# Kernel tuning notes

Measured on AMD Instinct MI355X. Metric: run time of the kernel, lower is better.

The kernel has to match this reference:

```python
import jax, jax.numpy as jnp
import numpy as np

N_NODES = 50000
NUM_FEATURE = 256
NUM_HIDDEN = 128
NUM_CLASSES = 16
N_EDGES = 1600000


def gcn_conv(x, W, b, src, dst, deg_inv_sqrt, n_nodes):
    # GCNConv: h = x @ W ; out[i] = sum_{j->i} norm_ji * h[j] + b
    # with symmetric normalization over the self-loop-augmented graph.
    h = x @ W  # [N, out_ch]
    norm = deg_inv_sqrt[src] * deg_inv_sqrt[dst]  # [E']
    msgs = h[src] * norm[:, None]  # [E', out_ch] (dominant intermediate)
    out = jax.ops.segment_sum(msgs, dst, num_segments=n_nodes)
    return out + b


def setup_inputs() -> dict:
    key = jax.random.key(0)
    k_x, k_e, k_w1, k_b1, k_w2, k_b2 = jax.random.split(key, 6)
    x = jax.random.normal(k_x, (N_NODES, NUM_FEATURE), dtype=jnp.float32)
    edge_index = jax.random.randint(k_e, (2, N_EDGES), 0, N_NODES, dtype=jnp.int64)
    # Glorot init like PyG's GCNConv linear
    s1 = (6.0 / (NUM_FEATURE + NUM_HIDDEN)) ** 0.5
    s2 = (6.0 / (NUM_HIDDEN + NUM_CLASSES)) ** 0.5
    W1 = jax.random.uniform(k_w1, (NUM_FEATURE, NUM_HIDDEN), jnp.float32, -s1, s1)
    b1 = jnp.zeros((NUM_HIDDEN,), jnp.float32)
    W2 = jax.random.uniform(k_w2, (NUM_HIDDEN, NUM_CLASSES), jnp.float32, -s2, s2)
    b2 = jnp.zeros((NUM_CLASSES,), jnp.float32)
    return {"x": x, "edge_index": edge_index, "W1": W1, "b1": b1, "W2": W2, "b2": b2}


def reference(x, edge_index, W1, b1, W2, b2):
    n = x.shape[0]
    # add self-loops (done inside GCNConv for each layer; identical both times)
    loops = jnp.arange(n, dtype=edge_index.dtype)
    src = jnp.concatenate([edge_index[0], loops])
    dst = jnp.concatenate([edge_index[1], loops])
    deg = jax.ops.segment_sum(jnp.ones_like(dst, dtype=x.dtype), dst, num_segments=n)
    deg_inv_sqrt = jnp.where(deg > 0, jax.lax.rsqrt(deg), 0.0)

    h = jax.nn.relu(gcn_conv(x, W1, b1, src, dst, deg_inv_sqrt, n))
    # F.dropout with training=False is the identity (eval-mode baseline)
    logits = gcn_conv(h, W2, b2, src, dst, deg_inv_sqrt, n)
    return jax.nn.log_softmax(logits, axis=1)
```

## Files before the change

kernel.cpp:

```cpp
#include <hip/hip_runtime.h>
#include <hip/hip_fp16.h>
#include <math.h>

#define NF 256
#define NH 128
#define NC 16
#define NB 391
#define NBLK 512

typedef __attribute__((ext_vector_type(8))) short bf16x8;
typedef __attribute__((ext_vector_type(4))) float f32x4;
typedef __attribute__((ext_vector_type(2))) float f32v2;

__device__ __forceinline__ unsigned f2b(float f) {
    unsigned u = __float_as_uint(f);
    return (u + 0x7FFFu + ((u >> 16) & 1u)) >> 16;
}
__device__ __forceinline__ unsigned packt(float a, float b) {
    return (__float_as_uint(a) >> 16) | (__float_as_uint(b) & 0xFFFF0000u);
}
union h2u { __half2 h; unsigned u; };
__device__ __forceinline__ __half2 uh(unsigned u) { h2u c; c.u = u; return c.h; }
__device__ __forceinline__ unsigned hu(__half2 h) { h2u c; c.h = h; return c.u; }

__global__ void prep_kernel(const int* __restrict__ dst, int* __restrict__ hist, int E,
                            const float* __restrict__ W1, unsigned short* __restrict__ W1T,
                            unsigned* __restrict__ h1c32, unsigned* __restrict__ h2sb,
                            int N) {
    __shared__ int h[NB];
    int b = blockIdx.x, tid = threadIdx.x;
    if (b < NBLK) {
        for (int i = tid; i < NB; i += 256) h[i] = 0;
        __syncthreads();
        int e0 = (int)((long long)b * E / NBLK), e1 = (int)((long long)(b + 1) * E / NBLK);
        for (int e = e0 + tid; e < e1; e += 256)
            atomicAdd(&h[dst[e] >> 7], 1);
        __syncthreads();
        for (int i = tid; i < NB; i += 256) hist[b * NB + i] = h[i];
    } else {
        int idx = (b - NBLK) * 256 + tid;
        int n = idx >> 8, k = idx & 255;
        W1T[n * 256 + k] = (unsigned short)f2b(W1[(size_t)k * NH + n]);
        if (idx < 32) {
            int q = idx >> 4, j = idx & 15;
            h1c32[(size_t)q * (N + 1) * 16 + (size_t)N * 16 + j] = 0u;
        } else if (idx < 40) {
            h2sb[(size_t)N * 8 + (idx - 32)] = 0u;
        }
    }
}

__global__ void scanR_kernel(const int* __restrict__ hist, int* __restrict__ bsum) {
    __shared__ int sm[NBLK];
    int k = blockIdx.x, t = threadIdx.x;
    sm[t] = hist[t * NB + k];
    __syncthreads();
    for (int off = NBLK / 2; off > 0; off >>= 1) {
        if (t < off) sm[t] += sm[t + off];
        __syncthreads();
    }
    if (t == 0) bsum[k] = sm[0];
}

__global__ void scanB_kernel(const int* __restrict__ bsum, int* __restrict__ ubase,
                             int* __restrict__ pbase, int N, int E) {
    __shared__ int smu[512];
    __shared__ int smp[512];
    int t = threadIdx.x;
    int vu = (t < NB) ? bsum[t] : 0;
    int vp = (t < NB) ? (((vu + 7) & ~7) + 904) : 0;
    smu[t] = vu; smp[t] = vp;
    __syncthreads();
    for (int off = 1; off < 512; off <<= 1) {
        int uu = (t >= off) ? smu[t - off] : 0;
        int pp = (t >= off) ? smp[t - off] : 0;
        __syncthreads();
        smu[t] += uu; smp[t] += pp;
        __syncthreads();
    }
    if (t < NB) { ubase[t] = smu[t] - vu; pbase[t] = smp[t] - vp; }
    if (t == 0) ubase[NB] = E;
}

__global__ void scanC_kernel(int* __restrict__ hist, const int* __restrict__ ubase) {
    __shared__ int sm[NBLK];
    int k = blockIdx.x, t = threadIdx.x;
    int v = hist[t * NB + k];
    sm[t] = v;
    __syncthreads();
    for (int off = 1; off < NBLK; off <<= 1) {
        int u = (t >= off) ? sm[t - off] : 0;
        __syncthreads();
        sm[t] += u;
        __syncthreads();
    }
    hist[t * NB + k] = ubase[k] + sm[t] - v;
}

__global__ void passB_kernel(const int* __restrict__ src, const int* __restrict__ dst,
                             const int* __restrict__ hist, unsigned* __restrict__ ebuf,
                             int E) {
    __shared__ int cur[NB];
    int b = blockIdx.x;
    for (int i = threadIdx.x; i < NB; i += 256) cur[i] = hist[b * NB + i];
    __syncthreads();
    int e0 = (int)((long long)b * E / NBLK), e1 = (int)((long long)(b + 1) * E / NBLK);
    for (int e = e0 + (int)threadIdx.x; e < e1; e += 256) {
        int d = dst[e];
        int pos = atomicAdd(&cur[d >> 7], 1);
        ebuf[pos] = ((unsigned)d << 16) | (unsigned)src[e];
    }
}

__global__ void passC_kernel(const unsigned* __restrict__ ebuf, const int* __restrict__ ubase,
                             const int* __restrict__ pbase, int* __restrict__ rowptr,
                             int* __restrict__ degs, float* __restrict__ dis,
                             unsigned short* __restrict__ colidx, int N) {
    __shared__ int h[128];
    __shared__ int s2[128];
    __shared__ int curp[128];
    int k = blockIdx.x, t = threadIdx.x;
    if (t < 128) h[t] = 0;
    __syncthreads();
    int e0 = ubase[k], e1 = ubase[k + 1];
    for (int e = e0 + t; e < e1; e += 256)
        atomicAdd(&h[(ebuf[e] >> 16) & 127], 1);
    __syncthreads();
    int v = (t < 128) ? h[t] : 0;
    int pd = (v + 7) & ~7;
    if (t < 128) s2[t] = pd;
    __syncthreads();
    for (int off = 1; off < 128; off <<= 1) {
        int u = (t < 128 && t >= off) ? s2[t - off] : 0;
        __syncthreads();
        if (t < 128) s2[t] += u;
        __syncthreads();
    }
    if (t < 128) {
        int start = pbase[k] + s2[t] - pd;
        int node = k * 128 + t;
        if (node < N) {
            rowptr[node] = start;
            degs[node] = v;
            dis[node] = rsqrtf((float)(v + 1));
        }
        curp[t] = start;
    }
    __syncthreads();
    for (int e = e0 + t; e < e1; e += 256) {
        unsigned w = ebuf[e];
        int dl = (w >> 16) & 127;
        int pos = atomicAdd(&curp[dl], 1);
        colidx[pos] = (unsigned short)(w & 0xFFFFu);
    }
    __syncthreads();
    if (t < 128) {
        int endp = pbase[k] + s2[t];
        for (int q = curp[t]; q < endp; ++q) colidx[q] = (unsigned short)N;
    }
}

__global__ __launch_bounds__(256) void gemm1_mfma_kernel(
    const float* __restrict__ x, const unsigned short* __restrict__ W1T,
    const float* __restrict__ dis, unsigned char* __restrict__ h1c, int N) {
    __shared__ char sx[32768];
    int tid = threadIdx.x;
    int wid = tid >> 6, lane = tid & 63;

    for (int it = 0; it < 8; ++it) {
        int lr = it * 4 + wid;
        int grow = blockIdx.x * 32 + lr;
        if (grow >= N) grow = N - 1;
        int fsw = (lr & 7) << 1;
        const char* gp = (const char*)x + (size_t)grow * 1024 + ((lane ^ fsw) << 4);
        __builtin_amdgcn_global_load_lds(gp, sx + lr * 1024 + lane * 16, 16, 0, 0);
    }
    __syncthreads();

    int lrow = lane & 15, lk = lane >> 4;
    int rt = wid & 1, nh = wid >> 1;
    int lr = rt * 16 + lrow;
    int fr = (lr & 7) << 1;
    const float4* lds4 = (const float4*)sx;

    bf16x8 a[8];
#pragma unroll
    for (int kk = 0; kk < 8; ++kk) {
        int v = (kk * 8 + lk * 2) ^ fr;
        float4 lo = lds4[lr * 64 + v];
        float4 hi = lds4[lr * 64 + v + 1];
        union { unsigned u[4]; bf16x8 vv; } av;
        av.u[0] = packt(lo.x, lo.y);
        av.u[1] = packt(lo.z, lo.w);
        av.u[2] = packt(hi.x, hi.y);
        av.u[3] = packt(hi.z, hi.w);
        a[kk] = av.vv;
    }

    f32x4 acc[4];
#pragma unroll
    for (int t = 0; t < 4; ++t) acc[t] = (f32x4){0.f, 0.f, 0.f, 0.f};

#pragma unroll
    for (int nt = 0; nt < 4; ++nt) {
        int n = nh * 64 + nt * 16 + lrow;
        const unsigned short* wp = W1T + (size_t)n * 256 + lk * 8;
        bf16x8 b0 = *(const bf16x8*)(wp + 0 * 32);
        bf16x8 b1 = *(const bf16x8*)(wp + 1 * 32);
        bf16x8 b2 = *(const bf16x8*)(wp + 2 * 32);
        bf16x8 b3 = *(const bf16x8*)(wp + 3 * 32);
        bf16x8 b4 = *(const bf16x8*)(wp + 4 * 32);
        bf16x8 b5 = *(const bf16x8*)(wp + 5 * 32);
        bf16x8 b6 = *(const bf16x8*)(wp + 6 * 32);
        bf16x8 b7 = *(const bf16x8*)(wp + 7 * 32);
        acc[nt] = __builtin_amdgcn_mfma_f32_16x16x32_bf16(a[0], b0, acc[nt], 0, 0, 0);
        acc[nt] = __builtin_amdgcn_mfma_f32_16x16x32_bf16(a[1], b1, acc[nt], 0, 0, 0);
        acc[nt] = __builtin_amdgcn_mfma_f32_16x16x32_bf16(a[2], b2, acc[nt], 0, 0, 0);
        acc[nt] = __builtin_amdgcn_mfma_f32_16x16x32_bf16(a[3], b3, acc[nt], 0, 0, 0);
        acc[nt] = __builtin_amdgcn_mfma_f32_16x16x32_bf16(a[4], b4, acc[nt], 0, 0, 0);
        acc[nt] = __builtin_amdgcn_mfma_f32_16x16x32_bf16(a[5], b5, acc[nt], 0, 0, 0);
        acc[nt] = __builtin_amdgcn_mfma_f32_16x16x32_bf16(a[6], b6, acc[nt], 0, 0, 0);
        acc[nt] = __builtin_amdgcn_mfma_f32_16x16x32_bf16(a[7], b7, acc[nt], 0, 0, 0);
    }

    int rb = blockIdx.x * 32;
    int crow0 = rb + rt * 16 + lk * 4;
#pragma unroll
    for (int r = 0; r < 4; ++r) {
        int row = crow0 + r;
        if (row < N) {
            float dr = dis[row];
            size_t base = ((size_t)nh * (N + 1) + row) * 64;
#pragma unroll
            for (int nt = 0; nt < 4; ++nt) {
                float v = acc[nt][r] * dr;
                int pk = __builtin_amdgcn_cvt_pk_fp8_f32(v, v, 0, 0);
                h1c[base + nt * 16 + lrow] = (unsigned char)(pk & 0xFF);
            }
        }
    }
}

__global__ __launch_bounds__(256) void aggall_kernel(
    const int* __restrict__ rowptr, const int* __restrict__ degs,
    const unsigned short* __restrict__ colidx,
    const unsigned char* __restrict__ h1c, __half2* __restrict__ aggT, int N, int bps) {
    int p = blockIdx.x / bps;
    int i = (blockIdx.x - p * bps) * 16 + (threadIdx.x >> 4);
    if (i >= N) return;
    int l = threadIdx.x & 15;
    const unsigned* slab = (const unsigned*)(h1c + (size_t)p * (N + 1) * 64);
    unsigned sv = slab[(size_t)i * 16 + l];
    f32v2 c0 = __builtin_amdgcn_cvt_pk_f32_fp8((int)sv, 0);
    f32v2 c1 = __builtin_amdgcn_cvt_pk_f32_fp8((int)sv, 1);
    float f0 = c0.x, f1 = c0.y, f2 = c1.x, f3 = c1.y;
    int e = rowptr[i];
    int cnt8 = (degs[i] + 7) >> 3;
    if (cnt8 > 0) {
        uint4 w = *reinterpret_cast<const uint4*>(colidx + e);
        for (int b = 1; b < cnt8; ++b) {
            uint4 wn = *reinterpret_cast<const uint4*>(colidx + e + 8 * b);
            int a0 = w.x & 0xFFFF, a1 = w.x >> 16, a2 = w.y & 0xFFFF, a3 = w.y >> 16;
            int a4 = w.z & 0xFFFF, a5 = w.z >> 16, a6 = w.w & 0xFFFF, a7 = w.w >> 16;
            unsigned g0 = slab[(size_t)a0 * 16 + l];
            unsigned g1 = slab[(size_t)a1 * 16 + l];
            unsigned g2 = slab[(size_t)a2 * 16 + l];
            unsigned g3 = slab[(size_t)a3 * 16 + l];
            unsigned g4 = slab[(size_t)a4 * 16 + l];
            unsigned g5 = slab[(size_t)a5 * 16 + l];
            unsigned g6 = slab[(size_t)a6 * 16 + l];
            unsigned g7 = slab[(size_t)a7 * 16 + l];
            f32v2 d;
            d = __builtin_amdgcn_cvt_pk_f32_fp8((int)g0, 0); f0 += d.x; f1 += d.y;
            d = __builtin_amdgcn_cvt_pk_f32_fp8((int)g0, 1); f2 += d.x; f3 += d.y;
            d = __builtin_amdgcn_cvt_pk_f32_fp8((int)g1, 0); f0 += d.x; f1 += d.y;
            d = __builtin_amdgcn_cvt_pk_f32_fp8((int)g1, 1); f2 += d.x; f3 += d.y;
            d = __builtin_amdgcn_cvt_pk_f32_fp8((int)g2, 0); f0 += d.x; f1 += d.y;
            d = __builtin_amdgcn_cvt_pk_f32_fp8((int)g2, 1); f2 += d.x; f3 += d.y;
            d = __builtin_amdgcn_cvt_pk_f32_fp8((int)g3, 0); f0 += d.x; f1 += d.y;
            d = __builtin_amdgcn_cvt_pk_f32_fp8((int)g3, 1); f2 += d.x; f3 += d.y;
            d = __builtin_amdgcn_cvt_pk_f32_fp8((int)g4, 0); f0 += d.x; f1 += d.y;
            d = __builtin_amdgcn_cvt_pk_f32_fp8((int)g4, 1); f2 += d.x; f3 += d.y;
            d = __builtin_amdgcn_cvt_pk_f32_fp8((int)g5, 0); f0 += d.x; f1 += d.y;
            d = __builtin_amdgcn_cvt_pk_f32_fp8((int)g5, 1); f2 += d.x; f3 += d.y;
            d = __builtin_amdgcn_cvt_pk_f32_fp8((int)g6, 0); f0 += d.x; f1 += d.y;
            d = __builtin_amdgcn_cvt_pk_f32_fp8((int)g6, 1); f2 += d.x; f3 += d.y;
            d = __builtin_amdgcn_cvt_pk_f32_fp8((int)g7, 0); f0 += d.x; f1 += d.y;
            d = __builtin_amdgcn_cvt_pk_f32_fp8((int)g7, 1); f2 += d.x; f3 += d.y;
            w = wn;
        }
        {
            int a0 = w.x & 0xFFFF, a1 = w.x >> 16, a2 = w.y & 0xFFFF, a3 = w.y >> 16;
            int a4 = w.z & 0xFFFF, a5 = w.z >> 16, a6 = w.w & 0xFFFF, a7 = w.w >> 16;
            unsigned g0 = slab[(size_t)a0 * 16 + l];
            unsigned g1 = slab[(size_t)a1 * 16 + l];
            unsigned g2 = slab[(size_t)a2 * 16 + l];
            unsigned g3 = slab[(size_t)a3 * 16 + l];
            unsigned g4 = slab[(size_t)a4 * 16 + l];
            unsigned g5 = slab[(size_t)a5 * 16 + l];
            unsigned g6 = slab[(size_t)a6 * 16 + l];
            unsigned g7 = slab[(size_t)a7 * 16 + l];
            f32v2 d;
            d = __builtin_amdgcn_cvt_pk_f32_fp8((int)g0, 0); f0 += d.x; f1 += d.y;
            d = __builtin_amdgcn_cvt_pk_f32_fp8((int)g0, 1); f2 += d.x; f3 += d.y;
            d = __builtin_amdgcn_cvt_pk_f32_fp8((int)g1, 0); f0 += d.x; f1 += d.y;
            d = __builtin_amdgcn_cvt_pk_f32_fp8((int)g1, 1); f2 += d.x; f3 += d.y;
            d = __builtin_amdgcn_cvt_pk_f32_fp8((int)g2, 0); f0 += d.x; f1 += d.y;
            d = __builtin_amdgcn_cvt_pk_f32_fp8((int)g2, 1); f2 += d.x; f3 += d.y;
            d = __builtin_amdgcn_cvt_pk_f32_fp8((int)g3, 0); f0 += d.x; f1 += d.y;
            d = __builtin_amdgcn_cvt_pk_f32_fp8((int)g3, 1); f2 += d.x; f3 += d.y;
            d = __builtin_amdgcn_cvt_pk_f32_fp8((int)g4, 0); f0 += d.x; f1 += d.y;
            d = __builtin_amdgcn_cvt_pk_f32_fp8((int)g4, 1); f2 += d.x; f3 += d.y;
            d = __builtin_amdgcn_cvt_pk_f32_fp8((int)g5, 0); f0 += d.x; f1 += d.y;
            d = __builtin_amdgcn_cvt_pk_f32_fp8((int)g5, 1); f2 += d.x; f3 += d.y;
            d = __builtin_amdgcn_cvt_pk_f32_fp8((int)g6, 0); f0 += d.x; f1 += d.y;
            d = __builtin_amdgcn_cvt_pk_f32_fp8((int)g6, 1); f2 += d.x; f3 += d.y;
            d = __builtin_amdgcn_cvt_pk_f32_fp8((int)g7, 0); f0 += d.x; f1 += d.y;
            d = __builtin_amdgcn_cvt_pk_f32_fp8((int)g7, 1); f2 += d.x; f3 += d.y;
        }
    }
    __half2 h01 = __floats2half2_rn(f0, f1);
    __half2 h23 = __floats2half2_rn(f2, f3);
    size_t base = ((size_t)(p * 2 + (l >> 3)) * N + i) * 16 + ((2 * l) & 15);
    *reinterpret_cast<uint2*>(aggT + base) = make_uint2(hu(h01), hu(h23));
}

__global__ __launch_bounds__(256) void relu_gemm2_kernel(
    const __half2* __restrict__ aggT, const float* __restrict__ dis,
    const float* __restrict__ b1, const float* __restrict__ W2,
    __half2* __restrict__ h2sb, int N) {
    __shared__ float sW2[NH * NC];
    __shared__ float srow[4][NH];
    int tid = threadIdx.x;
    for (int k = tid; k < NH * NC; k += 256) sW2[k] = W2[k];
    __syncthreads();

    int wid = tid >> 6, lane = tid & 63;
    int i = blockIdx.x * 4 + wid;
    if (i >= N) return;
    int p = lane >> 4, l16 = lane & 15;
    float2 f = __half22float2(aggT[((size_t)p * N + i) * 16 + l16]);
    float di = dis[i];
    int c0 = p * 32 + l16 * 2;
    srow[wid][c0]     = fmaxf(di * f.x + b1[c0], 0.f);
    srow[wid][c0 + 1] = fmaxf(di * f.y + b1[c0 + 1], 0.f);
    int j = lane & 15, q = lane >> 4;
    const float* rw = srow[wid];
    float pacc = 0.f;
#pragma unroll
    for (int cc = 0; cc < 32; ++cc) {
        int c = q * 32 + cc;
        pacc += rw[c] * sW2[c * NC + j];
    }
    pacc += __shfl_xor(pacc, 16, 64);
    pacc += __shfl_xor(pacc, 32, 64);
    float dp = di * pacc;
    float plo = __shfl(dp, (lane << 1) & 63, 64);
    float phi = __shfl(dp, ((lane << 1) | 1) & 63, 64);
    if (lane < 8) h2sb[(size_t)i * 8 + lane] = __floats2half2_rn(plo, phi);
}

__global__ void layer2_kernel(const int* __restrict__ rowptr, const int* __restrict__ degs,
                              const unsigned short* __restrict__ colidx,
                              const uint2* __restrict__ h2sb2, const float* __restrict__ dis,
                              const float* __restrict__ b2, float* __restrict__ out, int N) {
    int t = blockIdx.x * 256 + threadIdx.x;
    int i = t >> 2;
    if (i >= N) return;
    int j4 = t & 3;
    int e = rowptr[i];
    int cnt4 = (degs[i] + 3) >> 2;
    uint2 sv = h2sb2[(size_t)i * 4 + j4];
    __half2 acc0 = uh(sv.x), acc1 = uh(sv.y);
    if (cnt4 > 0) {
        uint2 w = *reinterpret_cast<const uint2*>(colidx + e);
        for (int b = 1; b < cnt4; ++b) {
            uint2 wn = *reinterpret_cast<const uint2*>(colidx + e + 4 * b);
            int a0 = w.x & 0xFFFF, a1 = w.x >> 16;
            int a2 = w.y & 0xFFFF, a3 = w.y >> 16;
            uint2 g0 = h2sb2[(size_t)a0 * 4 + j4];
            uint2 g1 = h2sb2[(size_t)a1 * 4 + j4];
            uint2 g2 = h2sb2[(size_t)a2 * 4 + j4];
            uint2 g3 = h2sb2[(size_t)a3 * 4 + j4];
            acc0 = __hadd2(acc0, __hadd2(__hadd2(uh(g0.x), uh(g1.x)),
                                         __hadd2(uh(g2.x), uh(g3.x))));
            acc1 = __hadd2(acc1, __hadd2(__hadd2(uh(g0.y), uh(g1.y)),
                                         __hadd2(uh(g2.y), uh(g3.y))));
            w = wn;
        }
        int a0 = w.x & 0xFFFF, a1 = w.x >> 16;
        int a2 = w.y & 0xFFFF, a3 = w.y >> 16;
        uint2 g0 = h2sb2[(size_t)a0 * 4 + j4];
        uint2 g1 = h2sb2[(size_t)a1 * 4 + j4];
        uint2 g2 = h2sb2[(size_t)a2 * 4 + j4];
        uint2 g3 = h2sb2[(size_t)a3 * 4 + j4];
        acc0 = __hadd2(acc0, __hadd2(__hadd2(uh(g0.x), uh(g1.x)),
                                     __hadd2(uh(g2.x), uh(g3.x))));
        acc1 = __hadd2(acc1, __hadd2(__hadd2(uh(g0.y), uh(g1.y)),
                                     __hadd2(uh(g2.y), uh(g3.y))));
    }
    float2 f0 = __half22float2(acc0);
    float2 f1 = __half22float2(acc1);
    float di = dis[i];
    float4 bb = *reinterpret_cast<const float4*>(b2 + 4 * j4);
    float l0 = di * f0.x + bb.x;
    float l1 = di * f0.y + bb.y;
    float l2 = di * f1.x + bb.z;
    float l3 = di * f1.y + bb.w;
    float m = fmaxf(fmaxf(l0, l1), fmaxf(l2, l3));
    m = fmaxf(m, __shfl_xor(m, 1, 64));
    m = fmaxf(m, __shfl_xor(m, 2, 64));
    float s = __expf(l0 - m) + __expf(l1 - m) + __expf(l2 - m) + __expf(l3 - m);
    s += __shfl_xor(s, 1, 64);
    s += __shfl_xor(s, 2, 64);
    float lse = m + __logf(s);
    float4 o = make_float4(l0 - lse, l1 - lse, l2 - lse, l3 - lse);
    *reinterpret_cast<float4*>(out + (size_t)i * NC + 4 * j4) = o;
}

extern "C" void kernel_launch(void* const* d_in, const int* in_sizes, int n_in,
                              void* d_out, int out_size, void* d_ws, size_t ws_size,
                              hipStream_t stream) {
    const float* x  = (const float*)d_in[0];
    const int*   ei = (const int*)d_in[1];
    const float* W1 = (const float*)d_in[2];
    const float* b1 = (const float*)d_in[3];
    const float* W2 = (const float*)d_in[4];
    const float* b2 = (const float*)d_in[5];
    float* out = (float*)d_out;

    const int N = in_sizes[0] / NF;
    const int E = in_sizes[1] / 2;
    const int* src = ei;
    const int* dst = ei + E;

    unsigned char*  h1c    = (unsigned char*)d_ws;
    __half2*        aggT   = (__half2*)(h1c + (size_t)2 * (N + 1) * 64);
    __half2*        h2sb   = aggT + (size_t)4 * N * 16;
    float*          dis    = (float*)(h2sb + (size_t)(N + 1) * 8);
    int*            degs   = (int*)(dis + N);
    int*            rowptr = degs + N;
    int*            hist   = rowptr + N;
    int*            bsum   = hist + NBLK * NB;
    int*            ubase  = bsum + NB;
    int*            pbase  = ubase + NB + 1;
    unsigned*       ebuf   = (unsigned*)(pbase + NB + 2);
    unsigned short* colidx = (unsigned short*)(ebuf + E);
    unsigned short* W1T    = colidx + (size_t)E + 360000;

    prep_kernel<<<NBLK + 128, 256, 0, stream>>>(dst, hist, E, W1, W1T,
                                                (unsigned*)h1c, (unsigned*)h2sb, N);
    scanR_kernel<<<NB, NBLK, 0, stream>>>(hist, bsum);
    scanB_kernel<<<1, 512, 0, stream>>>(bsum, ubase, pbase, N, E);
    scanC_kernel<<<NB, NBLK, 0, stream>>>(hist, ubase);
    passB_kernel<<<NBLK, 256, 0, stream>>>(src, dst, hist, ebuf, E);
    passC_kernel<<<NB, 256, 0, stream>>>(ebuf, ubase, pbase, rowptr, degs, dis, colidx, N);

    gemm1_mfma_kernel<<<(N + 31) / 32, 256, 0, stream>>>(x, W1T, dis, h1c, N);

    const int bps = (N + 15) / 16;
    aggall_kernel<<<2 * bps, 256, 0, stream>>>(rowptr, degs, colidx, h1c, aggT, N, bps);

    relu_gemm2_kernel<<<(N + 3) / 4, 256, 0, stream>>>(aggT, dis, b1, W2, h2sb, N);

    layer2_kernel<<<((size_t)N * 4 + 255) / 256, 256, 0, stream>>>(rowptr, degs, colidx,
                                                                   (const uint2*)h2sb, dis, b2, out, N);
}
```

Baseline: 144.1 us.

## Fuse layer-1 aggregation into ReLU/GEMM2 kernel and merge scan kernels

The separate FP8 gather-aggregation kernel and the ReLU+GEMM2 kernel are fused into one kernel, so the fp16 aggT intermediate is never written to or read back from global memory. To support this, h1c is changed from two per-half slabs to an interleaved 128-byte row layout. Each wavefront handles one node, with its two 32-lane halves taking alternate edges and combining partial sums through a cross-half shuffle. The scanB and scanC kernels are also merged into one, which removes a launch; each block recomputes its own prefix with a reduction. The trade-off is less parallelism per node (one wave instead of eight lane groups split across two slabs) and redundant prefix work in every scan block.

Result: slower. 148.7 us (+3.2%).

```diff
diff --git a/kernel.cpp b/kernel.cpp
--- a/kernel.cpp
+++ b/kernel.cpp
@@ -21,12 +21,11 @@
 }
 union h2u { __half2 h; unsigned u; };
 __device__ __forceinline__ __half2 uh(unsigned u) { h2u c; c.u = u; return c.h; }
-__device__ __forceinline__ unsigned hu(__half2 h) { h2u c; c.h = h; return c.u; }
 
 __global__ void prep_kernel(const int* __restrict__ dst, int* __restrict__ hist, int E,
                             const float* __restrict__ W1, unsigned short* __restrict__ W1T,
                             unsigned* __restrict__ h1c32, unsigned* __restrict__ h2sb,
-                            int N) {
+                            int* __restrict__ ubase, int N) {
     __shared__ int h[NB];
     int b = blockIdx.x, tid = threadIdx.x;
     if (b < NBLK) {
@@ -42,10 +41,11 @@
         int n = idx >> 8, k = idx & 255;
         W1T[n * 256 + k] = (unsigned short)f2b(W1[(size_t)k * NH + n]);
         if (idx < 32) {
-            int q = idx >> 4, j = idx & 15;
-            h1c32[(size_t)q * (N + 1) * 16 + (size_t)N * 16 + j] = 0u;
+            h1c32[(size_t)N * 32 + idx] = 0u;
         } else if (idx < 40) {
             h2sb[(size_t)N * 8 + (idx - 32)] = 0u;
+        } else if (idx == 40) {
+            ubase[NB] = E;
         }
     }
 }
@@ -62,39 +62,33 @@
     if (t == 0) bsum[k] = sm[0];
 }
 
-__global__ void scanB_kernel(const int* __restrict__ bsum, int* __restrict__ ubase,
-                             int* __restrict__ pbase, int N, int E) {
-    __shared__ int smu[512];
-    __shared__ int smp[512];
-    int t = threadIdx.x;
-    int vu = (t < NB) ? bsum[t] : 0;
-    int vp = (t < NB) ? (((vu + 7) & ~7) + 904) : 0;
-    smu[t] = vu; smp[t] = vp;
-    __syncthreads();
-    for (int off = 1; off < 512; off <<= 1) {
-        int uu = (t >= off) ? smu[t - off] : 0;
-        int pp = (t >= off) ? smp[t - off] : 0;
-        __syncthreads();
-        smu[t] += uu; smp[t] += pp;
-        __syncthreads();
-    }
-    if (t < NB) { ubase[t] = smu[t] - vu; pbase[t] = smp[t] - vp; }
-    if (t == 0) ubase[NB] = E;
-}
-
-__global__ void scanC_kernel(int* __restrict__ hist, const int* __restrict__ ubase) {
-    __shared__ int sm[NBLK];
+__global__ void scanCB_kernel(const int* __restrict__ bsum, int* __restrict__ hist,
+                              int* __restrict__ ubase, int* __restrict__ pbase) {
+    __shared__ int sr[NBLK];
+    __shared__ int sp[NBLK];
+    __shared__ int ubs;
     int k = blockIdx.x, t = threadIdx.x;
+    int vu = (t < k) ? bsum[t] : 0;
+    int vp = (t < k) ? (((vu + 7) & ~7) + 904) : 0;
+    sr[t] = vu; sp[t] = vp;
+    __syncthreads();
+    for (int off = NBLK / 2; off > 0; off >>= 1) {
+        if (t < off) { sr[t] += sr[t + off]; sp[t] += sp[t + off]; }
+        __syncthreads();
+    }
+    if (t == 0) { ubs = sr[0]; ubase[k] = sr[0]; pbase[k] = sp[0]; }
+    __syncthreads();
+    int ub = ubs;
     int v = hist[t * NB + k];
-    sm[t] = v;
+    sr[t] = v;
     __syncthreads();
     for (int off = 1; off < NBLK; off <<= 1) {
-        int u = (t >= off) ? sm[t - off] : 0;
-        __syncthreads();
-        sm[t] += u;
-        __syncthreads();
-    }
-    hist[t * NB + k] = ubase[k] + sm[t] - v;
+        int u = (t >= off) ? sr[t - off] : 0;
+        __syncthreads();
+        sr[t] += u;
+        __syncthreads();
+    }
+    hist[t * NB + k] = ub + sr[t] - v;
 }
 
 __global__ void passB_kernel(const int* __restrict__ src, const int* __restrict__ dst,
@@ -230,7 +224,7 @@
         int row = crow0 + r;
         if (row < N) {
             float dr = dis[row];
-            size_t base = ((size_t)nh * (N + 1) + row) * 64;
+            size_t base = (size_t)row * 128 + nh * 64;
 #pragma unroll
             for (int nt = 0; nt < 4; ++nt) {
                 float v = acc[nt][r] * dr;
@@ -241,92 +235,10 @@
     }
 }
 
-__global__ __launch_bounds__(256) void aggall_kernel(
+__global__ __launch_bounds__(256) void aggfused_kernel(
     const int* __restrict__ rowptr, const int* __restrict__ degs,
     const unsigned short* __restrict__ colidx,
-    const unsigned char* __restrict__ h1c, __half2* __restrict__ aggT, int N, int bps) {
-    int p = blockIdx.x / bps;
-    int i = (blockIdx.x - p * bps) * 16 + (threadIdx.x >> 4);
-    if (i >= N) return;
-    int l = threadIdx.x & 15;
-    const unsigned* slab = (const unsigned*)(h1c + (size_t)p * (N + 1) * 64);
-    unsigned sv = slab[(size_t)i * 16 + l];
-    f32v2 c0 = __builtin_amdgcn_cvt_pk_f32_fp8((int)sv, 0);
-    f32v2 c1 = __builtin_amdgcn_cvt_pk_f32_fp8((int)sv, 1);
-    float f0 = c0.x, f1 = c0.y, f2 = c1.x, f3 = c1.y;
-    int e = rowptr[i];
-    int cnt8 = (degs[i] + 7) >> 3;
-    if (cnt8 > 0) {
-        uint4 w = *reinterpret_cast<const uint4*>(colidx + e);
-        for (int b = 1; b < cnt8; ++b) {
-            uint4 wn = *reinterpret_cast<const uint4*>(colidx + e + 8 * b);
-            int a0 = w.x & 0xFFFF, a1 = w.x >> 16, a2 = w.y & 0xFFFF, a3 = w.y >> 16;
-            int a4 = w.z & 0xFFFF, a5 = w.z >> 16, a6 = w.w & 0xFFFF, a7 = w.w >> 16;
-            unsigned g0 = slab[(size_t)a0 * 16 + l];
-            unsigned g1 = slab[(size_t)a1 * 16 + l];
-            unsigned g2 = slab[(size_t)a2 * 16 + l];
-            unsigned g3 = slab[(size_t)a3 * 16 + l];
-            unsigned g4 = slab[(size_t)a4 * 16 + l];
-            unsigned g5 = slab[(size_t)a5 * 16 + l];
-            unsigned g6 = slab[(size_t)a6 * 16 + l];
-            unsigned g7 = slab[(size_t)a7 * 16 + l];
-            f32v2 d;
-            d = __builtin_amdgcn_cvt_pk_f32_fp8((int)g0, 0); f0 += d.x; f1 += d.y;
-            d = __builtin_amdgcn_cvt_pk_f32_fp8((int)g0, 1); f2 += d.x; f3 += d.y;
-            d = __builtin_amdgcn_cvt_pk_f32_fp8((int)g1, 0); f0 += d.x; f1 += d.y;
-            d = __builtin_amdgcn_cvt_pk_f32_fp8((int)g1, 1); f2 += d.x; f3 += d.y;
-            d = __builtin_amdgcn_cvt_pk_f32_fp8((int)g2, 0); f0 += d.x; f1 += d.y;
-            d = __builtin_amdgcn_cvt_pk_f32_fp8((int)g2, 1); f2 += d.x; f3 += d.y;
-            d = __builtin_amdgcn_cvt_pk_f32_fp8((int)g3, 0); f0 += d.x; f1 += d.y;
-            d = __builtin_amdgcn_cvt_pk_f32_fp8((int)g3, 1); f2 += d.x; f3 += d.y;
-            d = __builtin_amdgcn_cvt_pk_f32_fp8((int)g4, 0); f0 += d.x; f1 += d.y;
-            d = __builtin_amdgcn_cvt_pk_f32_fp8((int)g4, 1); f2 += d.x; f3 += d.y;
-            d = __builtin_amdgcn_cvt_pk_f32_fp8((int)g5, 0); f0 += d.x; f1 += d.y;
-            d = __builtin_amdgcn_cvt_pk_f32_fp8((int)g5, 1); f2 += d.x; f3 += d.y;
-            d = __builtin_amdgcn_cvt_pk_f32_fp8((int)g6, 0); f0 += d.x; f1 += d.y;
-            d = __builtin_amdgcn_cvt_pk_f32_fp8((int)g6, 1); f2 += d.x; f3 += d.y;
-            d = __builtin_amdgcn_cvt_pk_f32_fp8((int)g7, 0); f0 += d.x; f1 += d.y;
-            d = __builtin_amdgcn_cvt_pk_f32_fp8((int)g7, 1); f2 += d.x; f3 += d.y;
-            w = wn;
-        }
-        {
-            int a0 = w.x & 0xFFFF, a1 = w.x >> 16, a2 = w.y & 0xFFFF, a3 = w.y >> 16;
-            int a4 = w.z & 0xFFFF, a5 = w.z >> 16, a6 = w.w & 0xFFFF, a7 = w.w >> 16;
-            unsigned g0 = slab[(size_t)a0 * 16 + l];
-            unsigned g1 = slab[(size_t)a1 * 16 + l];
-            unsigned g2 = slab[(size_t)a2 * 16 + l];
-            unsigned g3 = slab[(size_t)a3 * 16 + l];
-            unsigned g4 = slab[(size_t)a4 * 16 + l];
-            unsigned g5 = slab[(size_t)a5 * 16 + l];
-            unsigned g6 = slab[(size_t)a6 * 16 + l];
-            unsigned g7 = slab[(size_t)a7 * 16 + l];
-            f32v2 d;
-            d = __builtin_amdgcn_cvt_pk_f32_fp8((int)g0, 0); f0 += d.x; f1 += d.y;
-            d = __builtin_amdgcn_cvt_pk_f32_fp8((int)g0, 1); f2 += d.x; f3 += d.y;
-            d = __builtin_amdgcn_cvt_pk_f32_fp8((int)g1, 0); f0 += d.x; f1 += d.y;
-            d = __builtin_amdgcn_cvt_pk_f32_fp8((int)g1, 1); f2 += d.x; f3 += d.y;
-            d = __builtin_amdgcn_cvt_pk_f32_fp8((int)g2, 0); f0 += d.x; f1 += d.y;
-            d = __builtin_amdgcn_cvt_pk_f32_fp8((int)g2, 1); f2 += d.x; f3 += d.y;
-            d = __builtin_amdgcn_cvt_pk_f32_fp8((int)g3, 0); f0 += d.x; f1 += d.y;
-            d = __builtin_amdgcn_cvt_pk_f32_fp8((int)g3, 1); f2 += d.x; f3 += d.y;
-            d = __builtin_amdgcn_cvt_pk_f32_fp8((int)g4, 0); f0 += d.x; f1 += d.y;
-            d = __builtin_amdgcn_cvt_pk_f32_fp8((int)g4, 1); f2 += d.x; f3 += d.y;
-            d = __builtin_amdgcn_cvt_pk_f32_fp8((int)g5, 0); f0 += d.x; f1 += d.y;
-            d = __builtin_amdgcn_cvt_pk_f32_fp8((int)g5, 1); f2 += d.x; f3 += d.y;
-            d = __builtin_amdgcn_cvt_pk_f32_fp8((int)g6, 0); f0 += d.x; f1 += d.y;
-            d = __builtin_amdgcn_cvt_pk_f32_fp8((int)g6, 1); f2 += d.x; f3 += d.y;
-            d = __builtin_amdgcn_cvt_pk_f32_fp8((int)g7, 0); f0 += d.x; f1 += d.y;
-            d = __builtin_amdgcn_cvt_pk_f32_fp8((int)g7, 1); f2 += d.x; f3 += d.y;
-        }
-    }
-    __half2 h01 = __floats2half2_rn(f0, f1);
-    __half2 h23 = __floats2half2_rn(f2, f3);
-    size_t base = ((size_t)(p * 2 + (l >> 3)) * N + i) * 16 + ((2 * l) & 15);
-    *reinterpret_cast<uint2*>(aggT + base) = make_uint2(hu(h01), hu(h23));
-}
-
-__global__ __launch_bounds__(256) void relu_gemm2_kernel(
-    const __half2* __restrict__ aggT, const float* __restrict__ dis,
+    const unsigned* __restrict__ h1c32, const float* __restrict__ dis,
     const float* __restrict__ b1, const float* __restrict__ W2,
     __half2* __restrict__ h2sb, int N) {
     __shared__ float sW2[NH * NC];
@@ -338,19 +250,69 @@
     int wid = tid >> 6, lane = tid & 63;
     int i = blockIdx.x * 4 + wid;
     if (i >= N) return;
-    int p = lane >> 4, l16 = lane & 15;
-    float2 f = __half22float2(aggT[((size_t)p * N + i) * 16 + l16]);
+    int c = lane & 31;
+    int half = lane >> 5;
+
+    unsigned sv = h1c32[(size_t)i * 32 + c];
+    float f0 = 0.f, f1 = 0.f, f2 = 0.f, f3 = 0.f;
+    int e = rowptr[i];
+    int steps = ((degs[i] + 7) >> 3) * 2;
+    const unsigned* cidx32 = (const unsigned*)colidx;
+    int w0i = e >> 1;
+    if (steps > 0) {
+        uint2 w = *(const uint2*)(cidx32 + w0i);
+        for (int s = 1; s < steps; ++s) {
+            uint2 wn = *(const uint2*)(cidx32 + w0i + 2 * s);
+            int aA = half ? (int)(w.x >> 16) : (int)(w.x & 0xFFFFu);
+            int aB = half ? (int)(w.y >> 16) : (int)(w.y & 0xFFFFu);
+            unsigned gA = h1c32[(size_t)aA * 32 + c];
+            unsigned gB = h1c32[(size_t)aB * 32 + c];
+            f32v2 dA0 = __builtin_amdgcn_cvt_pk_f32_fp8((int)gA, 0);
+            f32v2 dA1 = __builtin_amdgcn_cvt_pk_f32_fp8((int)gA, 1);
+            f32v2 dB0 = __builtin_amdgcn_cvt_pk_f32_fp8((int)gB, 0);
+            f32v2 dB1 = __builtin_amdgcn_cvt_pk_f32_fp8((int)gB, 1);
+            f0 += dA0.x + dB0.x; f1 += dA0.y + dB0.y;
+            f2 += dA1.x + dB1.x; f3 += dA1.y + dB1.y;
+            w = wn;
+        }
+        {
+            int aA = half ? (int)(w.x >> 16) : (int)(w.x & 0xFFFFu);
+            int aB = half ? (int)(w.y >> 16) : (int)(w.y & 0xFFFFu);
+            unsigned gA = h1c32[(size_t)aA * 32 + c];
+            unsigned gB = h1c32[(size_t)aB * 32 + c];
+            f32v2 dA0 = __builtin_amdgcn_cvt_pk_f32_fp8((int)gA, 0);
+            f32v2 dA1 = __builtin_amdgcn_cvt_pk_f32_fp8((int)gA, 1);
+            f32v2 dB0 = __builtin_amdgcn_cvt_pk_f32_fp8((int)gB, 0);
+            f32v2 dB1 = __builtin_amdgcn_cvt_pk_f32_fp8((int)gB, 1);
+            f0 += dA0.x + dB0.x; f1 += dA0.y + dB0.y;
+            f2 += dA1.x + dB1.x; f3 += dA1.y + dB1.y;
+        }
+    }
+    if (half == 0) {
+        f32v2 s0 = __builtin_amdgcn_cvt_pk_f32_fp8((int)sv, 0);
+        f32v2 s1 = __builtin_amdgcn_cvt_pk_f32_fp8((int)sv, 1);
+        f0 += s0.x; f1 += s0.y; f2 += s1.x; f3 += s1.y;
+    }
+    f0 += __shfl_xor(f0, 32, 64);
+    f1 += __shfl_xor(f1, 32, 64);
+    f2 += __shfl_xor(f2, 32, 64);
+    f3 += __shfl_xor(f3, 32, 64);
+
     float di = dis[i];
-    int c0 = p * 32 + l16 * 2;
-    srow[wid][c0]     = fmaxf(di * f.x + b1[c0], 0.f);
-    srow[wid][c0 + 1] = fmaxf(di * f.y + b1[c0 + 1], 0.f);
+    if (half == 0) {
+        int c0 = c * 4;
+        srow[wid][c0 + 0] = fmaxf(di * f0 + b1[c0 + 0], 0.f);
+        srow[wid][c0 + 1] = fmaxf(di * f1 + b1[c0 + 1], 0.f);
+        srow[wid][c0 + 2] = fmaxf(di * f2 + b1[c0 + 2], 0.f);
+        srow[wid][c0 + 3] = fmaxf(di * f3 + b1[c0 + 3], 0.f);
+    }
     int j = lane & 15, q = lane >> 4;
     const float* rw = srow[wid];
     float pacc = 0.f;
 #pragma unroll
     for (int cc = 0; cc < 32; ++cc) {
-        int c = q * 32 + cc;
-        pacc += rw[c] * sW2[c * NC + j];
+        int c2 = q * 32 + cc;
+        pacc += rw[c2] * sW2[c2 * NC + j];
     }
     pacc += __shfl_xor(pacc, 16, 64);
     pacc += __shfl_xor(pacc, 32, 64);
@@ -435,8 +397,7 @@
     const int* dst = ei + E;
 
     unsigned char*  h1c    = (unsigned char*)d_ws;
-    __half2*        aggT   = (__half2*)(h1c + (size_t)2 * (N + 1) * 64);
-    __half2*        h2sb   = aggT + (size_t)4 * N * 16;
+    __half2*        h2sb   = (__half2*)(h1c + (size_t)(N + 1) * 128);
     float*          dis    = (float*)(h2sb + (size_t)(N + 1) * 8);
     int*            degs   = (int*)(dis + N);
     int*            rowptr = degs + N;
@@ -449,19 +410,18 @@
     unsigned short* W1T    = colidx + (size_t)E + 360000;
 
     prep_kernel<<<NBLK + 128, 256, 0, stream>>>(dst, hist, E, W1, W1T,
-                                                (unsigned*)h1c, (unsigned*)h2sb, N);
+                                                (unsigned*)h1c, (unsigned*)h2sb,
+                                                ubase, N);
     scanR_kernel<<<NB, NBLK, 0, stream>>>(hist, bsum);
-    scanB_kernel<<<1, 512, 0, stream>>>(bsum, ubase, pbase, N, E);
-    scanC_kernel<<<NB, NBLK, 0, stream>>>(hist, ubase);
+    scanCB_kernel<<<NB, NBLK, 0, stream>>>(bsum, hist, ubase, pbase);
     passB_kernel<<<NBLK, 256, 0, stream>>>(src, dst, hist, ebuf, E);
     passC_kernel<<<NB, 256, 0, stream>>>(ebuf, ubase, pbase, rowptr, degs, dis, colidx, N);
 
     gemm1_mfma_kernel<<<(N + 31) / 32, 256, 0, stream>>>(x, W1T, dis, h1c, N);
 
-    const int bps = (N + 15) / 16;
-    aggall_kernel<<<2 * bps, 256, 0, stream>>>(rowptr, degs, colidx, h1c, aggT, N, bps);
-
-    relu_gemm2_kernel<<<(N + 3) / 4, 256, 0, stream>>>(aggT, dis, b1, W2, h2sb, N);
+    aggfused_kernel<<<(N + 3) / 4, 256, 0, stream>>>(rowptr, degs, colidx,
+                                                     (const unsigned*)h1c, dis, b1, W2,
+                                                     h2sb, N);
 
     layer2_kernel<<<((size_t)N * 4 + 255) / 256, 256, 0, stream>>>(rowptr, degs, colidx,
                                                                    (const uint2*)h2sb, dis, b2, out, N);
```
